# Kernel tuning notes

Hardware: AMD Instinct MI355X
Metric: run time of the kernel (lower is better)

## Reference

```python
import jax, jax.numpy as jnp
import numpy as np
import math

B, N, D = 2, 4096, 1024
NUM_LAYERS = 12
INIT_RANGE = 0.02


def setup_inputs() -> dict:
    key = jax.random.key(0)
    k1, k2 = jax.random.split(key)
    hidden_states = jax.random.normal(k1, (B, N, D), dtype=jnp.float32)
    std = INIT_RANGE / math.sqrt(2.0 * NUM_LAYERS * D)
    queries = jax.random.normal(k2, (D, D), dtype=jnp.float32) * std
    return {"hidden_states": hidden_states, "queries": queries}


def reference(hidden_states, queries):
    # Q = F.linear(X, W) = X @ W^T  -> [B, N, D]
    q = jnp.einsum('bnd,ed->bne', hidden_states, queries)
    # pre_attn = Q @ X^T  -> [B, N, N]
    pre_attn = jnp.einsum('bne,bme->bnm', q, hidden_states)
    # attention = pre_attn @ X  -> [B, N, D]
    attention = jnp.einsum('bnm,bmd->bnd', pre_attn, hidden_states)
    return attention
```

## Files before the change

### kernel.cpp

```cpp
#include <hip/hip_runtime.h>
#include <hip/hip_bf16.h>
#include <stdint.h>

using bf16 = __hip_bfloat16;
typedef __attribute__((ext_vector_type(8))) short short8;
typedef __attribute__((ext_vector_type(4))) float f32x4;

#define BM 128
#define BK 32

__device__ __forceinline__ void g2lds16(const void* g, void* l) {
    __builtin_amdgcn_global_load_lds(
        (const __attribute__((address_space(1))) void*)g,
        (__attribute__((address_space(3))) void*)l,
        16, 0, 0);
}

template <int N>
__device__ __forceinline__ void s_wait_vmcnt() {
    asm volatile("s_waitcnt vmcnt(%0)" :: "n"(N) : "memory");
}

__device__ __forceinline__ short f2bs(float x) {
    union { bf16 h; short s; } u;
    u.h = __float2bfloat16(x);
    return u.s;
}

__device__ __forceinline__ int bswz(int row, int cg) { return cg ^ ((row >> 1) & 3); }
__device__ __forceinline__ int fswz(int row, int cg) { return cg ^ (row & 7); }

__global__ __launch_bounds__(256)
void transpose_cvt(const float* __restrict__ src, ushort* __restrict__ dstT,
                   ushort* __restrict__ dstN,
                   int R, int C, long sstride, long dstrideT, long dstrideN)
{
    __shared__ __align__(16) ushort t[64][72];
    const float* s = src + (size_t)blockIdx.z * sstride;
    ushort*      dT = dstT + (size_t)blockIdx.z * dstrideT;
    const int r0 = blockIdx.y * 64, c0 = blockIdx.x * 64;
    const int tid = threadIdx.x;
#pragma unroll
    for (int ii = 0; ii < 4; ++ii) {
        int idx = ii * 256 + tid;
        int r = idx >> 4, c4 = (idx & 15) * 4;
        float4 v = *(const float4*)&s[(size_t)(r0 + r) * C + c0 + c4];
        union { ushort u[4]; uint2 q; } o;
        o.u[0] = (ushort)f2bs(v.x); o.u[1] = (ushort)f2bs(v.y);
        o.u[2] = (ushort)f2bs(v.z); o.u[3] = (ushort)f2bs(v.w);
        *(uint2*)&t[r][c4] = o.q;
        if (dstN) {
            ushort* dN = dstN + (size_t)blockIdx.z * dstrideN;
            *(uint2*)&dN[(size_t)(r0 + r) * C + c0 + c4] = o.q;
        }
    }
    __syncthreads();
#pragma unroll
    for (int ii = 0; ii < 2; ++ii) {
        int idx = ii * 256 + tid;
        int c = idx >> 3, r8 = (idx & 7) * 8;
        union { ushort u[8]; uint4 v; } tmp;
#pragma unroll
        for (int j = 0; j < 8; ++j) tmp.u[j] = t[r8 + j][c];
        *(uint4*)&dT[(size_t)(c0 + c) * R + r0 + r8] = tmp.v;
    }
}

template <int MODE, int A_F32, int NFRAG>
__global__ __launch_bounds__(256)
void gemm_bt(const void* __restrict__ Av, const bf16* __restrict__ B,
             void* __restrict__ Cv, int M, int N, int K, int kChunks,
             long sA, long sB, long sC)
{
    constexpr int BN  = 32 * NFRAG;
    constexpr int BSH = (BN * BK * 2) / (256 * 16);
    constexpr int ASH = A_F32 ? 4 : 2;
    constexpr int L   = ASH + BSH;
    constexpr int ANE = BM * BK * (A_F32 ? 2 : 1);
    constexpr int BNE = BN * BK;
    __shared__ __align__(16) bf16 lA[3][ANE];
    __shared__ __align__(16) bf16 lB[3][BNE];

    const int gx   = gridDim.x, gy = gridDim.y;
    const int nwg  = gx * gy * gridDim.z;
    const int wgid = (blockIdx.z * gy + blockIdx.y) * gx + blockIdx.x;
    const int lid  = (wgid & 7) * (nwg >> 3) + (wgid >> 3);
    const int pz   = gx * gy;
    const int z    = lid / pz;
    const int rem  = lid - z * pz;
    const int my   = rem / gx;
    const int m0   = my * BM;
    const int n0   = (rem - my * gx) * BN;

    const int batch = z / kChunks;
    const int chunk = z - batch * kChunks;
    const int kLen  = K / kChunks;
    const int k0    = chunk * kLen;

    const int tid  = threadIdx.x;
    const int lane = tid & 63;
    const int wave = tid >> 6;
    const int wr   = wave >> 1, wc = wave & 1;
    const int ml   = lane & 15;
    const int q    = lane >> 4;

    const bf16* Bb = B + (size_t)batch * sB;
    const bf16* bp[BSH];
#pragma unroll
    for (int s = 0; s < BSH; ++s) {
        int idx = s * 256 + tid;
        int row = idx >> 2, cg = idx & 3;
        bp[s] = Bb + (size_t)(n0 + row) * K + k0 + 8 * bswz(row, cg);
    }

    const float* a32[4];
    const bf16*  a16[2];
    if constexpr (A_F32) {
        const float* Ab = (const float*)Av + (size_t)batch * sA;
#pragma unroll
        for (int s = 0; s < 4; ++s) {
            int idx = s * 256 + tid;
            int row = idx >> 3, cg = idx & 7;
            a32[s] = Ab + (size_t)(m0 + row) * K + k0 + 4 * fswz(row, cg);
        }
    } else {
        const bf16* Ab = (const bf16*)Av + (size_t)batch * sA;
#pragma unroll
        for (int s = 0; s < 2; ++s) {
            int idx = s * 256 + tid;
            int row = idx >> 2, cg = idx & 3;
            a16[s] = Ab + (size_t)(m0 + row) * K + k0 + 8 * bswz(row, cg);
        }
    }

    f32x4 acc[4][NFRAG] = {};

    auto stage = [&](int buf) {
        if constexpr (A_F32) {
            float* lAf = (float*)lA[buf];
#pragma unroll
            for (int s = 0; s < 4; ++s) {
                g2lds16(a32[s], &lAf[(s * 256 + tid) * 4]);
                a32[s] += BK;
            }
        } else {
#pragma unroll
            for (int s = 0; s < 2; ++s) {
                g2lds16(a16[s], &lA[buf][(s * 256 + tid) * 8]);
                a16[s] += BK;
            }
        }
#pragma unroll
        for (int s = 0; s < BSH; ++s) {
            g2lds16(bp[s], &lB[buf][(s * 256 + tid) * 8]);
            bp[s] += BK;
        }
    };

    auto frags = [&](int buf, short8 (&af)[4], short8 (&bfr)[NFRAG]) {
        const bf16* cA = lA[buf];
        const bf16* cB = lB[buf];
#pragma unroll
        for (int i = 0; i < 4; ++i) {
            const int rA = wr * 64 + i * 16 + ml;
            if constexpr (A_F32) {
                const float* lAf = (const float*)cA;
                float4 x0 = *(const float4*)&lAf[rA * 32 + 4 * fswz(rA, 2 * q)];
                float4 x1 = *(const float4*)&lAf[rA * 32 + 4 * fswz(rA, 2 * q + 1)];
                af[i][0] = f2bs(x0.x); af[i][1] = f2bs(x0.y);
                af[i][2] = f2bs(x0.z); af[i][3] = f2bs(x0.w);
                af[i][4] = f2bs(x1.x); af[i][5] = f2bs(x1.y);
                af[i][6] = f2bs(x1.z); af[i][7] = f2bs(x1.w);
            } else {
                af[i] = *(const short8*)&cA[rA * 32 + 8 * bswz(rA, q)];
            }
        }
#pragma unroll
        for (int j = 0; j < NFRAG; ++j) {
            const int rB = wc * (16 * NFRAG) + j * 16 + ml;
            bfr[j] = *(const short8*)&cB[rB * 32 + 8 * bswz(rB, q)];
        }
    };

    auto mfma = [&](short8 (&af)[4], short8 (&bfr)[NFRAG]) {
#pragma unroll
        for (int mi = 0; mi < 4; ++mi)
#pragma unroll
            for (int nj = 0; nj < NFRAG; ++nj)
                acc[mi][nj] = __builtin_amdgcn_mfma_f32_16x16x32_bf16(
                    af[mi], bfr[nj], acc[mi][nj], 0, 0, 0);
    };

    const int nk = kLen / BK;
    stage(0); stage(1);
    int cur = 0;
    for (int t = 0; t < nk - 2; ++t) {
        s_wait_vmcnt<L>();
        __builtin_amdgcn_s_barrier();
        short8 af_[4], bf_[NFRAG];
        frags(cur, af_, bf_);
        int nb = cur + 2; nb = (nb >= 3) ? nb - 3 : nb;
        stage(nb);
        mfma(af_, bf_);
        asm volatile("s_waitcnt lgkmcnt(0)" ::: "memory");
        cur = (cur == 2) ? 0 : cur + 1;
    }
    {
        s_wait_vmcnt<L>();
        __builtin_amdgcn_s_barrier();
        short8 af_[4], bf_[NFRAG];
        frags(cur, af_, bf_);
        mfma(af_, bf_);
        cur = (cur == 2) ? 0 : cur + 1;
    }
    {
        s_wait_vmcnt<0>();
        __builtin_amdgcn_s_barrier();
        short8 af_[4], bf_[NFRAG];
        frags(cur, af_, bf_);
        mfma(af_, bf_);
    }

#pragma unroll
    for (int mi = 0; mi < 4; ++mi)
#pragma unroll
        for (int nj = 0; nj < NFRAG; ++nj)
#pragma unroll
            for (int r = 0; r < 4; ++r) {
                int row = m0 + wr * 64 + mi * 16 + q * 4 + r;
                int col = n0 + wc * (16 * NFRAG) + nj * 16 + ml;
                if constexpr (MODE == 1) {
                    float* Cf = (float*)Cv + (size_t)batch * sC;
                    atomicAdd(&Cf[(size_t)row * N + col], acc[mi][nj][r]);
                } else if constexpr (MODE == 0) {
                    ushort* Cb = (ushort*)Cv + (size_t)batch * sC;
                    Cb[(size_t)row * N + col] = (ushort)f2bs(acc[mi][nj][r]);
                } else {
                    float* Cf = (float*)Cv + (size_t)batch * sC;
                    Cf[(size_t)row * N + col] = acc[mi][nj][r];
                }
            }
}

extern "C" void kernel_launch(void* const* d_in, const int* in_sizes, int n_in,
                              void* d_out, int out_size, void* d_ws, size_t ws_size,
                              hipStream_t stream)
{
    const int B = 2, N = 4096, D = 1024;
    const float* X = (const float*)d_in[0];
    const float* W = (const float*)d_in[1];
    float* out = (float*)d_out;

    char* ob = (char*)d_out;
    char* ws = (char*)d_ws;
    ushort* Xt = (ushort*)ob;
    float*  Gf = (float*)(ob + (16ll << 20));
    ushort* Wt = (ushort*)(ob + (28ll << 20));

    const bool bigws = ws_size >= (20ull << 20);
    ushort* Xb = bigws ? (ushort*)ws : nullptr;
    ushort* Mt = (ushort*)(ws + (bigws ? (16ll << 20) : 0));

    transpose_cvt<<<dim3(D / 64, N / 64, B), 256, 0, stream>>>(
        X, Xt, Xb, N, D, (long)N * D, (long)D * N, (long)N * D);
    transpose_cvt<<<dim3(D / 64, D / 64, 1), 256, 0, stream>>>(
        W, Wt, nullptr, D, D, 0, 0, 0);
    (void)hipMemsetAsync(Gf, 0, (size_t)B * D * D * sizeof(float), stream);
    gemm_bt<1, 0, 4><<<dim3(D / 128, D / BM, B * 4), 256, 0, stream>>>(
        (const void*)Xt, (const bf16*)Xt, Gf, D, D, N, 4,
        (long)D * N, (long)D * N, (long)D * D);
    gemm_bt<0, 1, 2><<<dim3(D / 64, D / BM, B), 256, 0, stream>>>(
        (const void*)Gf, (const bf16*)Wt, Mt, D, D, D, 1,
        (long)D * D, 0, (long)D * D);
    if (bigws) {
        gemm_bt<2, 0, 4><<<dim3(D / 128, N / BM, B), 256, 0, stream>>>(
            (const void*)Xb, (const bf16*)Mt, out, N, D, D, 1,
            (long)N * D, (long)D * D, (long)N * D);
    } else {
        gemm_bt<2, 1, 4><<<dim3(D / 128, N / BM, B), 256, 0, stream>>>(
            (const void*)X, (const bf16*)Mt, out, N, D, D, 1,
            (long)N * D, (long)D * D, (long)N * D);
    }
}
```

Measured before the change: 175.4 us.

## Add 256x256 tiled 512-thread GEMM kernel and bf16 pre-conversion of Gram matrix

Adds a new gemm256 kernel with 256x256 output tiles, 8 waves, double-buffered direct-to-LDS loads interleaved with MFMA phases, priority hints and XCD-aware block remapping. The three GEMM stages (X^T X Gram, G*W, X*M) now use it. A separate conversion pass turns the fp32 Gram matrix into bf16 first, so the second GEMM no longer converts fp32 A tiles on the fly. Larger tiles raise arithmetic intensity per LDS load, but they also produce far fewer workgroups (e.g. 32 for the G*W stage) and add an extra conversion launch. The small-workspace fallback also switches to the 64-wide gemm_bt variant.

```diff
diff --git a/kernel.cpp b/kernel.cpp
--- a/kernel.cpp
+++ b/kernel.cpp
@@ -64,6 +64,141 @@
         for (int j = 0; j < 8; ++j) tmp.u[j] = t[r8 + j][c];
         *(uint4*)&dT[(size_t)(c0 + c) * R + r0 + r8] = tmp.v;
     }
+}
+
+__global__ __launch_bounds__(256)
+void cvt_f32_bf16(const float* __restrict__ in, ushort* __restrict__ out, int n4)
+{
+    int i = blockIdx.x * 256 + threadIdx.x;
+    if (i >= n4) return;
+    float4 v = ((const float4*)in)[i];
+    union { ushort u[4]; uint2 q; } o;
+    o.u[0] = (ushort)f2bs(v.x); o.u[1] = (ushort)f2bs(v.y);
+    o.u[2] = (ushort)f2bs(v.z); o.u[3] = (ushort)f2bs(v.w);
+    ((uint2*)out)[i] = o.q;
+}
+
+template <int MODE>
+__global__ __launch_bounds__(512)
+void gemm256(const bf16* __restrict__ A, const bf16* __restrict__ B,
+             void* __restrict__ Cv, int M, int N, int K, int kChunks,
+             long sA, long sB, long sC)
+{
+    __shared__ __align__(16) bf16 lA[2][2][256 * 32];
+    __shared__ __align__(16) bf16 lB[2][2][256 * 32];
+
+    const int gx = gridDim.x, gy = gridDim.y;
+    const int nwg = gx * gy * gridDim.z;
+    const int wgid = (blockIdx.z * gy + blockIdx.y) * gx + blockIdx.x;
+    const int lid = (wgid & 7) * (nwg >> 3) + (wgid >> 3);
+    const int pz = gx * gy;
+    const int z = lid / pz;
+    const int rem = lid - z * pz;
+    const int my = rem / gx;
+    const int m0 = my * 256;
+    const int n0 = (rem - my * gx) * 256;
+
+    const int batch = z / kChunks;
+    const int chunk = z - batch * kChunks;
+    const int kLen = K / kChunks;
+    const int k0 = chunk * kLen;
+
+    const int tid = threadIdx.x;
+    const int lane = tid & 63;
+    const int wave = tid >> 6;
+    const int wm = wave >> 2, wn = wave & 3;
+    const int ml = lane & 15;
+    const int q = lane >> 4;
+
+    const bf16* Ab = A + (size_t)batch * sA;
+    const bf16* Bb = B + (size_t)batch * sB;
+    const int srow = tid >> 2, scg = tid & 3;
+    const bf16* pA[4];
+    const bf16* pB[4];
+#pragma unroll
+    for (int kk = 0; kk < 2; ++kk)
+#pragma unroll
+        for (int hh = 0; hh < 2; ++hh) {
+            int r = hh * 128 + srow;
+            long koff = k0 + kk * 32 + 8 * bswz(r, scg);
+            pA[kk * 2 + hh] = Ab + (size_t)(m0 + r) * K + koff;
+            pB[kk * 2 + hh] = Bb + (size_t)(n0 + r) * K + koff;
+        }
+
+    f32x4 acc[8][4] = {};
+
+    auto stageA = [&](int nbuf, int sh) {
+        g2lds16(pA[sh], &lA[nbuf][sh >> 1][(sh & 1) * 4096 + tid * 8]);
+        pA[sh] += 64;
+    };
+    auto stageB = [&](int nbuf, int sh) {
+        g2lds16(pB[sh], &lB[nbuf][sh >> 1][(sh & 1) * 4096 + tid * 8]);
+        pB[sh] += 64;
+    };
+
+    const int nk = kLen / 64;
+#pragma unroll
+    for (int sh = 0; sh < 4; ++sh) stageA(0, sh);
+#pragma unroll
+    for (int sh = 0; sh < 4; ++sh) stageB(0, sh);
+
+    for (int t = 0; t < nk; ++t) {
+        const int buf = t & 1;
+        const int nbuf = buf ^ 1;
+        const bool pf = (t + 1 < nk);
+        s_wait_vmcnt<0>();
+        __builtin_amdgcn_s_barrier();
+#pragma unroll
+        for (int p = 0; p < 4; ++p) {
+            const int qm = p >> 1, kk = p & 1;
+            short8 af[4], bf[4];
+#pragma unroll
+            for (int mf = 0; mf < 4; ++mf) {
+                int r = wm * 128 + qm * 64 + mf * 16 + ml;
+                af[mf] = *(const short8*)&lA[buf][kk][r * 32 + 8 * bswz(r, q)];
+            }
+#pragma unroll
+            for (int nf = 0; nf < 4; ++nf) {
+                int r = wn * 64 + nf * 16 + ml;
+                bf[nf] = *(const short8*)&lB[buf][kk][r * 32 + 8 * bswz(r, q)];
+            }
+            if (pf) {
+                if (p < 2) { stageA(nbuf, 2 * p); stageA(nbuf, 2 * p + 1); }
+                else       { stageB(nbuf, 2 * (p - 2)); stageB(nbuf, 2 * (p - 2) + 1); }
+            }
+            asm volatile("s_waitcnt lgkmcnt(0)" ::: "memory");
+            __builtin_amdgcn_sched_barrier(0);
+            __builtin_amdgcn_s_setprio(1);
+#pragma unroll
+            for (int mf = 0; mf < 4; ++mf)
+#pragma unroll
+                for (int nf = 0; nf < 4; ++nf)
+                    acc[qm * 4 + mf][nf] = __builtin_amdgcn_mfma_f32_16x16x32_bf16(
+                        af[mf], bf[nf], acc[qm * 4 + mf][nf], 0, 0, 0);
+            __builtin_amdgcn_s_setprio(0);
+            __builtin_amdgcn_s_barrier();
+        }
+    }
+
+#pragma unroll
+    for (int mi = 0; mi < 8; ++mi)
+#pragma unroll
+        for (int nf = 0; nf < 4; ++nf)
+#pragma unroll
+            for (int rr = 0; rr < 4; ++rr) {
+                int row = m0 + wm * 128 + (mi >> 2) * 64 + (mi & 3) * 16 + q * 4 + rr;
+                int col = n0 + wn * 64 + nf * 16 + ml;
+                if constexpr (MODE == 1) {
+                    float* Cf = (float*)Cv + (size_t)batch * sC;
+                    atomicAdd(&Cf[(size_t)row * N + col], acc[mi][nf][rr]);
+                } else if constexpr (MODE == 0) {
+                    ushort* Cb = (ushort*)Cv + (size_t)batch * sC;
+                    Cb[(size_t)row * N + col] = (ushort)f2bs(acc[mi][nf][rr]);
+                } else {
+                    float* Cf = (float*)Cv + (size_t)batch * sC;
+                    Cf[(size_t)row * N + col] = acc[mi][nf][rr];
+                }
+            }
 }
 
 template <int MODE, int A_F32, int NFRAG>
@@ -255,6 +390,7 @@
     char* ws = (char*)d_ws;
     ushort* Xt = (ushort*)ob;
     float*  Gf = (float*)(ob + (16ll << 20));
+    ushort* Gb = (ushort*)(ob + (24ll << 20));
     ushort* Wt = (ushort*)(ob + (28ll << 20));
 
     const bool bigws = ws_size >= (20ull << 20);
@@ -266,18 +402,20 @@
     transpose_cvt<<<dim3(D / 64, D / 64, 1), 256, 0, stream>>>(
         W, Wt, nullptr, D, D, 0, 0, 0);
     (void)hipMemsetAsync(Gf, 0, (size_t)B * D * D * sizeof(float), stream);
-    gemm_bt<1, 0, 4><<<dim3(D / 128, D / BM, B * 4), 256, 0, stream>>>(
-        (const void*)Xt, (const bf16*)Xt, Gf, D, D, N, 4,
+    gemm256<1><<<dim3(D / 256, D / 256, B * 4), 512, 0, stream>>>(
+        (const bf16*)Xt, (const bf16*)Xt, Gf, D, D, N, 4,
         (long)D * N, (long)D * N, (long)D * D);
-    gemm_bt<0, 1, 2><<<dim3(D / 64, D / BM, B), 256, 0, stream>>>(
-        (const void*)Gf, (const bf16*)Wt, Mt, D, D, D, 1,
+    cvt_f32_bf16<<<dim3(B * D * D / 4 / 256), 256, 0, stream>>>(
+        Gf, Gb, B * D * D / 4);
+    gemm256<0><<<dim3(D / 256, D / 256, B), 512, 0, stream>>>(
+        (const bf16*)Gb, (const bf16*)Wt, Mt, D, D, D, 1,
         (long)D * D, 0, (long)D * D);
     if (bigws) {
-        gemm_bt<2, 0, 4><<<dim3(D / 128, N / BM, B), 256, 0, stream>>>(
-            (const void*)Xb, (const bf16*)Mt, out, N, D, D, 1,
+        gemm256<2><<<dim3(D / 256, N / 256, B), 512, 0, stream>>>(
+            (const bf16*)Xb, (const bf16*)Mt, out, N, D, D, 1,
             (long)N * D, (long)D * D, (long)N * D);
     } else {
-        gemm_bt<2, 1, 4><<<dim3(D / 128, N / BM, B), 256, 0, stream>>>(
+        gemm_bt<2, 1, 2><<<dim3(D / 64, N / BM, B), 256, 0, stream>>>(
             (const void*)X, (const bf16*)Mt, out, N, D, D, 1,
             (long)N * D, (long)D * D, (long)N * D);
     }
```

New measurement: 207.9 us. +18.5%, slower.
